# Optimization experiments

Measured on AMD Instinct MI355X. Metric: run time of the kernel, lower is better.

## Reference

```python
import jax, jax.numpy as jnp
import numpy as np

B, S, D_IN, D_OUT = 8, 2048, 1024, 64

def setup_inputs() -> dict:
    key = jax.random.key(0)
    ks = jax.random.split(key, 6)
    return {
        "inputs_for_keys": jax.random.normal(ks[0], (B, S, D_IN), jnp.float32),
        "inputs_for_values": jax.random.normal(ks[1], (B, S, D_IN), jnp.float32),
        "inputs_for_queries": jax.random.normal(ks[2], (B, S, D_IN), jnp.float32),
        "K": jax.random.normal(ks[3], (D_IN, D_OUT), jnp.float32) * (1.0 / np.sqrt(D_IN)),
        "V": jax.random.normal(ks[4], (D_IN, D_OUT), jnp.float32) * (1.0 / np.sqrt(D_IN)),
        "Q": jax.random.normal(ks[5], (D_IN, D_OUT), jnp.float32) * (1.0 / np.sqrt(D_IN)),
    }

def reference(inputs_for_keys, inputs_for_values, inputs_for_queries, K, V, Q):
    # Project to per-head key/value/query spaces: [B, S, D_OUT]
    keys = jnp.einsum('bsd,de->bse', inputs_for_keys, K)
    values = jnp.einsum('bsd,de->bse', inputs_for_values, V)
    queries = jnp.einsum('bsd,de->bse', inputs_for_queries, Q)
    d_k = keys.shape[-1]
    # Scaled dot-product scores: [B, Sq, Sk]
    score = jnp.einsum('bqe,bke->bqk', queries, keys) / jnp.sqrt(jnp.float32(d_k))
    # Causal mask: -inf strictly above the diagonal (query i attends to keys <= i)
    sq, sk = score.shape[1], score.shape[2]
    causal = jnp.triu(jnp.full((sq, sk), -jnp.inf, dtype=score.dtype), k=1)
    score = score + causal[None, :, :]
    weights = jax.nn.softmax(score, axis=-1)
    # Attention output: [B, Sq, D_OUT]
    return jnp.einsum('bqk,bke->bqe', weights, values)
```

## Files before the change

kernel.cpp:

```cpp
#include <hip/hip_runtime.h>
#include <stdint.h>

#define BB   8
#define SS   2048
#define DIN  1024
#define DOUT 64

typedef __bf16 bf16_t;
typedef __bf16 bf16x4 __attribute__((ext_vector_type(4)));
typedef __bf16 bf16x8 __attribute__((ext_vector_type(8)));
typedef float  f32x4  __attribute__((ext_vector_type(4)));
typedef unsigned int u32x4 __attribute__((ext_vector_type(4)));

#define LOG2E 1.44269504088896f

__device__ __forceinline__ void load_lds16(const void* g, void* l) {
    __builtin_amdgcn_global_load_lds(
        (const __attribute__((address_space(1))) void*)g,
        (__attribute__((address_space(3))) void*)l, 16, 0, 0);
}

__global__ void prep_weights(const float* __restrict__ Kw,
                             const float* __restrict__ Vw,
                             const float* __restrict__ Qw,
                             bf16_t* __restrict__ fw) {
    int proj = blockIdx.x >> 4;
    int seg  = blockIdx.x & 15;
    const float* W = (proj == 0) ? Kw : (proj == 1) ? Vw : Qw;
    float scale = (proj == 2) ? 0.125f : 1.0f;
    bf16_t* out = fw + proj * 65536;
    int base = seg * 4096;
#pragma unroll
    for (int i = 0; i < 16; ++i) {
        int idx  = base + i * 256 + threadIdx.x;
        int j    = idx & 7;
        int lane = (idx >> 3) & 63;
        int nt   = (idx >> 9) & 3;
        int kk   = idx >> 11;
        int k    = kk * 32 + (lane >> 4) * 8 + j;
        int col  = nt * 16 + (lane & 15);
        out[idx] = (bf16_t)(W[k * DOUT + col] * scale);
    }
}

__global__ __launch_bounds__(256) void proj_kernel(
    const float* __restrict__ Xk, const float* __restrict__ Xv,
    const float* __restrict__ Xq, const bf16_t* __restrict__ fw,
    bf16_t* __restrict__ outK, bf16_t* __restrict__ outVT,
    bf16_t* __restrict__ outQ) {
    __shared__ __align__(128) char Al[8192];
    __shared__ __align__(128) char Bl[8192];

    int tid  = threadIdx.x;
    int lane = tid & 63;
    int w    = tid >> 6;

    int proj = blockIdx.y;
    const float* X  = (proj == 0) ? Xk : (proj == 1) ? Xv : Xq;
    bf16_t* out     = (proj == 0) ? outK : (proj == 1) ? outVT : outQ;
    const bf16_t* fwp = fw + proj * 65536;

    int row0 = blockIdx.x * 32;

    const float* ga = X + (size_t)(row0 + (tid >> 4)) * DIN + ((tid & 15) ^ (tid >> 4)) * 4;
    char* alds0 = Al + (w << 10);
    char* alds1 = Al + 4096 + (w << 10);
    char* blds0 = Bl + (w << 10);
    char* blds1 = Bl + 4096 + (w << 10);

    f32x4 acc0 = (f32x4)(0.0f), acc1 = (f32x4)(0.0f);
    int r   = (w & 1) * 16 + (lane & 15);
    int nt0 = (w >> 1) * 2;

    for (int kt = 0; kt < 16; ++kt) {
        load_lds16(ga + kt * 64,               alds0);
        load_lds16(ga + 16 * DIN + kt * 64,    alds1);
        load_lds16(fwp + kt * 4096 + tid * 8,        blds0);
        load_lds16(fwp + kt * 4096 + 2048 + tid * 8, blds1);
        __syncthreads();

#pragma unroll
        for (int s = 0; s < 2; ++s) {
            int b0 = s * 8 + (lane >> 4) * 2;
            f32x4 lo = *(const f32x4*)(Al + r * 256 + (((b0    ) ^ (lane & 15)) << 4));
            f32x4 hi = *(const f32x4*)(Al + r * 256 + (((b0 + 1) ^ (lane & 15)) << 4));
            bf16x8 af;
            af[0] = (bf16_t)lo[0]; af[1] = (bf16_t)lo[1];
            af[2] = (bf16_t)lo[2]; af[3] = (bf16_t)lo[3];
            af[4] = (bf16_t)hi[0]; af[5] = (bf16_t)hi[1];
            af[6] = (bf16_t)hi[2]; af[7] = (bf16_t)hi[3];
            bf16x8 bf0 = *(const bf16x8*)(Bl + s * 4096 + nt0 * 1024 + lane * 16);
            bf16x8 bf1 = *(const bf16x8*)(Bl + s * 4096 + (nt0 + 1) * 1024 + lane * 16);
            acc0 = __builtin_amdgcn_mfma_f32_16x16x32_bf16(af, bf0, acc0, 0, 0, 0);
            acc1 = __builtin_amdgcn_mfma_f32_16x16x32_bf16(af, bf1, acc1, 0, 0, 0);
        }
        __syncthreads();
    }

    if (proj != 1) {
#pragma unroll
        for (int j = 0; j < 4; ++j) {
            int orow = row0 + (w & 1) * 16 + (lane >> 4) * 4 + j;
            out[(size_t)orow * DOUT + nt0 * 16 + (lane & 15)]       = (bf16_t)acc0[j];
            out[(size_t)orow * DOUT + (nt0 + 1) * 16 + (lane & 15)] = (bf16_t)acc1[j];
        }
    } else {
#pragma unroll
        for (int j = 0; j < 4; ++j) {
            int row = (w & 1) * 16 + (lane >> 4) * 4 + j;
            int c0  = nt0 * 16 + (lane & 15);
            int c1  = c0 + 16;
            *(bf16_t*)(Al + row * 128 + ((c0 * 2) ^ ((row & 7) << 4))) = (bf16_t)acc0[j];
            *(bf16_t*)(Al + row * 128 + ((c1 * 2) ^ ((row & 7) << 4))) = (bf16_t)acc1[j];
        }
        __syncthreads();
        int b  = row0 >> 11;
        int s0 = row0 & 2047;
        int sl = tid & 31;
        int d0 = (tid >> 5) * 8;
        bf16_t vals[8];
#pragma unroll
        for (int j = 0; j < 8; ++j)
            vals[j] = *(const bf16_t*)(Al + sl * 128 + (((d0 + j) * 2) ^ ((sl & 7) << 4)));
#pragma unroll
        for (int j = 0; j < 8; ++j)
            out[(size_t)b * (DOUT * SS) + (size_t)(d0 + j) * SS + s0 + sl] = vals[j];
    }
}

__global__ __launch_bounds__(256) void attn_kernel(
    const bf16_t* __restrict__ Kp, const bf16_t* __restrict__ VpT,
    const bf16_t* __restrict__ Qp, float* __restrict__ out,
    float* __restrict__ Opart, float* __restrict__ Oml, int split) {
    __shared__ __align__(16) char Plds[4][2048];

    int tid  = threadIdx.x;
    int lane = tid & 63;
    int w    = tid >> 6;
    int idx  = blockIdx.x;
    int b    = blockIdx.y;

    int qt, t0, t1, half = 0;
    bool partial;
    if (!split || idx < 16) { qt = idx; t0 = 0; t1 = qt + 1; partial = false; }
    else {
        int e = idx - 16;
        qt   = 16 + (e >> 1);
        half = e & 1;
        int T = qt + 1, h = (T + 1) >> 1;
        t0 = half ? h : 0;
        t1 = half ? T : h;
        partial = true;
    }

    const bf16_t* Kb = Kp  + (size_t)b * SS * DOUT;
    const bf16_t* Vb = VpT + (size_t)b * DOUT * SS;
    const bf16_t* Qb = Qp  + (size_t)b * SS * DOUT;

    bf16x8 aq0, aq1;
    {
        int rq = qt * 64 + w * 16 + (lane & 15);
        const bf16_t* qp = Qb + (size_t)rq * DOUT + (lane >> 4) * 8;
        aq0 = *(const bf16x8*)(qp);
        aq1 = *(const bf16x8*)(qp + 32);
    }

    float m[4], lsum[4];
    f32x4 acc[4];
#pragma unroll
    for (int r = 0; r < 4; ++r) { m[r] = -1e30f; lsum[r] = 0.0f; }
#pragma unroll
    for (int nt = 0; nt < 4; ++nt) acc[nt] = (f32x4)(0.0f);

    char* Pw = &Plds[w][0];

    for (int t = t0; t < t1; ++t) {
        f32x4 sfr[4];
#pragma unroll
        for (int nt = 0; nt < 4; ++nt) sfr[nt] = (f32x4)(0.0f);
#pragma unroll
        for (int kk = 0; kk < 2; ++kk) {
            int d0 = kk * 32 + (lane >> 4) * 8;
#pragma unroll
            for (int nt = 0; nt < 4; ++nt) {
                int key = nt * 16 + (lane & 15);
                bf16x8 bk = *(const bf16x8*)(Kb + (size_t)(t * 64 + key) * DOUT + d0);
                sfr[nt] = __builtin_amdgcn_mfma_f32_16x16x32_bf16(
                              kk == 0 ? aq0 : aq1, bk, sfr[nt], 0, 0, 0);
            }
        }

        if (t == qt) {
#pragma unroll
            for (int nt = 0; nt < 4; ++nt) {
                int key = nt * 16 + (lane & 15);
#pragma unroll
                for (int r = 0; r < 4; ++r) {
                    int q = w * 16 + (lane >> 4) * 4 + r;
                    if (key > q) sfr[nt][r] = -1e30f;
                }
            }
        }

        float pf[4][4];
#pragma unroll
        for (int r = 0; r < 4; ++r) {
            float mx = fmaxf(fmaxf(sfr[0][r], sfr[1][r]), fmaxf(sfr[2][r], sfr[3][r]));
            mx = fmaxf(mx, __shfl_xor(mx, 1));
            mx = fmaxf(mx, __shfl_xor(mx, 2));
            mx = fmaxf(mx, __shfl_xor(mx, 4));
            mx = fmaxf(mx, __shfl_xor(mx, 8));
            float mn = fmaxf(m[r], mx);
            float scale = exp2f((m[r] - mn) * LOG2E);
            m[r] = mn;
            float rs = 0.0f;
#pragma unroll
            for (int nt = 0; nt < 4; ++nt) {
                float p = exp2f((sfr[nt][r] - mn) * LOG2E);
                pf[nt][r] = p;
                rs += p;
            }
            rs += __shfl_xor(rs, 1);
            rs += __shfl_xor(rs, 2);
            rs += __shfl_xor(rs, 4);
            rs += __shfl_xor(rs, 8);
            lsum[r] = lsum[r] * scale + rs;
#pragma unroll
            for (int nt = 0; nt < 4; ++nt) acc[nt][r] *= scale;
        }

#pragma unroll
        for (int nt = 0; nt < 4; ++nt) {
            int key = nt * 16 + (lane & 15);
#pragma unroll
            for (int r = 0; r < 4; ++r) {
                int q = (lane >> 4) * 4 + r;
                *(bf16_t*)(Pw + q * 128 + ((key * 2) ^ ((q & 7) << 4))) = (bf16_t)pf[nt][r];
            }
        }

#pragma unroll
        for (int kk = 0; kk < 2; ++kk) {
            int k0 = kk * 32 + (lane >> 4) * 8;
            int q  = lane & 15;
            bf16x8 ap = *(const bf16x8*)(Pw + q * 128 + ((k0 * 2) ^ ((q & 7) << 4)));
#pragma unroll
            for (int nt = 0; nt < 4; ++nt) {
                int d = nt * 16 + (lane & 15);
                bf16x8 bv = *(const bf16x8*)(Vb + (size_t)d * SS + t * 64 + k0);
                acc[nt] = __builtin_amdgcn_mfma_f32_16x16x32_bf16(ap, bv, acc[nt], 0, 0, 0);
            }
        }
    }

    if (!partial) {
        float* ob = out + ((size_t)b * SS + qt * 64 + w * 16) * DOUT;
#pragma unroll
        for (int nt = 0; nt < 4; ++nt)
#pragma unroll
            for (int r = 0; r < 4; ++r) {
                int q = (lane >> 4) * 4 + r;
                int d = nt * 16 + (lane & 15);
                ob[(size_t)q * DOUT + d] = acc[nt][r] / lsum[r];
            }
    } else {
        size_t pbase = (((size_t)b * 16 + (qt - 16)) * 2 + half);
        float* Op = Opart + pbase * 4096;
        float* Ml = Oml   + pbase * 128;
#pragma unroll
        for (int nt = 0; nt < 4; ++nt)
#pragma unroll
            for (int r = 0; r < 4; ++r) {
                int row = w * 16 + (lane >> 4) * 4 + r;
                Op[row * 64 + nt * 16 + (lane & 15)] = acc[nt][r];
            }
        if ((lane & 15) == 0) {
#pragma unroll
            for (int r = 0; r < 4; ++r) {
                int row = w * 16 + (lane >> 4) * 4 + r;
                Ml[row * 2]     = m[r];
                Ml[row * 2 + 1] = lsum[r];
            }
        }
    }
}

__global__ __launch_bounds__(256) void attn_combine(
    const float* __restrict__ Opart, const float* __restrict__ Oml,
    float* __restrict__ out) {
    int qt  = 16 + blockIdx.x;
    int b   = blockIdx.y;
    int tid = threadIdx.x;
    int row = tid >> 2;
    int cb  = (tid & 3) * 16;

    size_t base = ((size_t)b * 16 + (qt - 16)) * 2;
    const float* O0 = Opart + base * 4096;
    const float* O1 = O0 + 4096;
    const float* M0 = Oml + base * 128;
    const float* M1 = M0 + 128;

    float m0 = M0[row * 2], l0 = M0[row * 2 + 1];
    float m1 = M1[row * 2], l1 = M1[row * 2 + 1];
    float mm = fmaxf(m0, m1);
    float e0 = exp2f((m0 - mm) * LOG2E);
    float e1 = exp2f((m1 - mm) * LOG2E);
    float li = 1.0f / (l0 * e0 + l1 * e1);

    const float* p0 = O0 + row * 64 + cb;
    const float* p1 = O1 + row * 64 + cb;
    float* ob = out + ((size_t)b * SS + qt * 64 + row) * DOUT + cb;
#pragma unroll
    for (int i = 0; i < 4; ++i) {
        f32x4 a = *(const f32x4*)(p0 + i * 4);
        f32x4 c = *(const f32x4*)(p1 + i * 4);
        f32x4 o;
#pragma unroll
        for (int j = 0; j < 4; ++j) o[j] = (a[j] * e0 + c[j] * e1) * li;
        *(f32x4*)(ob + i * 4) = o;
    }
}

extern "C" void kernel_launch(void* const* d_in, const int* in_sizes, int n_in,
                              void* d_out, int out_size, void* d_ws, size_t ws_size,
                              hipStream_t stream) {
    const float* Xk = (const float*)d_in[0];
    const float* Xv = (const float*)d_in[1];
    const float* Xq = (const float*)d_in[2];
    const float* Kw = (const float*)d_in[3];
    const float* Vw = (const float*)d_in[4];
    const float* Qw = (const float*)d_in[5];

    bf16_t* Kp  = (bf16_t*)d_ws;
    bf16_t* VpT = Kp  + (size_t)BB * SS * DOUT;
    bf16_t* Qp  = VpT + (size_t)BB * SS * DOUT;
    bf16_t* fw  = Qp  + (size_t)BB * SS * DOUT;
    char*   pend = (char*)(fw + 3 * 65536);
    float*  Opart = (float*)pend;
    float*  Oml   = Opart + (size_t)8 * 16 * 2 * 4096;

    size_t need = (size_t)((char*)(Oml + 8 * 16 * 2 * 128) - (char*)d_ws);
    int split = (ws_size >= need) ? 1 : 0;

    prep_weights<<<dim3(48), dim3(256), 0, stream>>>(Kw, Vw, Qw, fw);
    proj_kernel<<<dim3(512, 3), dim3(256), 0, stream>>>(Xk, Xv, Xq, fw, Kp, VpT, Qp);
    attn_kernel<<<dim3(split ? 48 : 32, 8), dim3(256), 0, stream>>>(
        Kp, VpT, Qp, (float*)d_out, Opart, Oml, split);
    if (split)
        attn_combine<<<dim3(16, 8), dim3(256), 0, stream>>>(Opart, Oml, (float*)d_out);
}
```

Before: 107.7 us.

## Triple-buffer projection GEMM LDS loads with manual vmcnt waits

Replaces the single-buffered load/sync/compute loop in the projection kernel with a 3-stage LDS ring buffer. Loads for tile t+2 are issued while tile t is computed, and explicit s_waitcnt vmcnt counts plus raw barriers replace __syncthreads. The goal is to hide global-memory latency of the fp32 activation stream behind the MFMA work. LDS use grows from 16KB to 48KB per block, which may reduce occupancy, and the hand-coded vmcnt values must match the number of outstanding loads.

```diff
diff --git a/kernel.cpp b/kernel.cpp
--- a/kernel.cpp
+++ b/kernel.cpp
@@ -48,8 +48,8 @@
     const float* __restrict__ Xq, const bf16_t* __restrict__ fw,
     bf16_t* __restrict__ outK, bf16_t* __restrict__ outVT,
     bf16_t* __restrict__ outQ) {
-    __shared__ __align__(128) char Al[8192];
-    __shared__ __align__(128) char Bl[8192];
+    __shared__ __align__(128) char Ab[3][8192];
+    __shared__ __align__(128) char Bb[3][8192];
 
     int tid  = threadIdx.x;
     int lane = tid & 63;
@@ -63,39 +63,51 @@
     int row0 = blockIdx.x * 32;
 
     const float* ga = X + (size_t)(row0 + (tid >> 4)) * DIN + ((tid & 15) ^ (tid >> 4)) * 4;
-    char* alds0 = Al + (w << 10);
-    char* alds1 = Al + 4096 + (w << 10);
-    char* blds0 = Bl + (w << 10);
-    char* blds1 = Bl + 4096 + (w << 10);
 
     f32x4 acc0 = (f32x4)(0.0f), acc1 = (f32x4)(0.0f);
     int r   = (w & 1) * 16 + (lane & 15);
     int nt0 = (w >> 1) * 2;
 
-    for (int kt = 0; kt < 16; ++kt) {
-        load_lds16(ga + kt * 64,               alds0);
-        load_lds16(ga + 16 * DIN + kt * 64,    alds1);
-        load_lds16(fwp + kt * 4096 + tid * 8,        blds0);
-        load_lds16(fwp + kt * 4096 + 2048 + tid * 8, blds1);
-        __syncthreads();
-
-#pragma unroll
-        for (int s = 0; s < 2; ++s) {
-            int b0 = s * 8 + (lane >> 4) * 2;
-            f32x4 lo = *(const f32x4*)(Al + r * 256 + (((b0    ) ^ (lane & 15)) << 4));
-            f32x4 hi = *(const f32x4*)(Al + r * 256 + (((b0 + 1) ^ (lane & 15)) << 4));
-            bf16x8 af;
-            af[0] = (bf16_t)lo[0]; af[1] = (bf16_t)lo[1];
-            af[2] = (bf16_t)lo[2]; af[3] = (bf16_t)lo[3];
-            af[4] = (bf16_t)hi[0]; af[5] = (bf16_t)hi[1];
-            af[6] = (bf16_t)hi[2]; af[7] = (bf16_t)hi[3];
-            bf16x8 bf0 = *(const bf16x8*)(Bl + s * 4096 + nt0 * 1024 + lane * 16);
-            bf16x8 bf1 = *(const bf16x8*)(Bl + s * 4096 + (nt0 + 1) * 1024 + lane * 16);
-            acc0 = __builtin_amdgcn_mfma_f32_16x16x32_bf16(af, bf0, acc0, 0, 0, 0);
-            acc1 = __builtin_amdgcn_mfma_f32_16x16x32_bf16(af, bf1, acc1, 0, 0, 0);
-        }
-        __syncthreads();
-    }
+#define STAGE(kt, b) do {                                                   \
+        load_lds16(ga + (kt) * 64,            Ab[b] + (w << 10));           \
+        load_lds16(ga + 16 * DIN + (kt) * 64, Ab[b] + 4096 + (w << 10));    \
+        load_lds16(fwp + (kt) * 4096 + tid * 8,        Bb[b] + (w << 10));  \
+        load_lds16(fwp + (kt) * 4096 + 2048 + tid * 8, Bb[b] + 4096 + (w << 10)); \
+    } while (0)
+
+#define COMPUTE(b) do {                                                     \
+        _Pragma("unroll")                                                   \
+        for (int s = 0; s < 2; ++s) {                                       \
+            int b0 = s * 8 + (lane >> 4) * 2;                               \
+            f32x4 lo = *(const f32x4*)(Ab[b] + r * 256 + (((b0    ) ^ (lane & 15)) << 4)); \
+            f32x4 hi = *(const f32x4*)(Ab[b] + r * 256 + (((b0 + 1) ^ (lane & 15)) << 4)); \
+            bf16x8 af;                                                      \
+            af[0] = (bf16_t)lo[0]; af[1] = (bf16_t)lo[1];                   \
+            af[2] = (bf16_t)lo[2]; af[3] = (bf16_t)lo[3];                   \
+            af[4] = (bf16_t)hi[0]; af[5] = (bf16_t)hi[1];                   \
+            af[6] = (bf16_t)hi[2]; af[7] = (bf16_t)hi[3];                   \
+            bf16x8 bf0 = *(const bf16x8*)(Bb[b] + s * 4096 + nt0 * 1024 + lane * 16); \
+            bf16x8 bf1 = *(const bf16x8*)(Bb[b] + s * 4096 + (nt0 + 1) * 1024 + lane * 16); \
+            acc0 = __builtin_amdgcn_mfma_f32_16x16x32_bf16(af, bf0, acc0, 0, 0, 0); \
+            acc1 = __builtin_amdgcn_mfma_f32_16x16x32_bf16(af, bf1, acc1, 0, 0, 0); \
+        }                                                                   \
+    } while (0)
+
+    STAGE(0, 0);
+    STAGE(1, 1);
+
+#pragma unroll
+    for (int t = 0; t < 16; ++t) {
+        if (t + 2 < 16) STAGE(t + 2, (t + 2) % 3);
+        if (t < 14)       asm volatile("s_waitcnt vmcnt(8)" ::: "memory");
+        else if (t == 14) asm volatile("s_waitcnt vmcnt(4)" ::: "memory");
+        else              asm volatile("s_waitcnt vmcnt(0)" ::: "memory");
+        __builtin_amdgcn_s_barrier();
+        COMPUTE(t % 3);
+        __builtin_amdgcn_s_barrier();
+    }
+#undef STAGE
+#undef COMPUTE
 
     if (proj != 1) {
 #pragma unroll
@@ -105,6 +117,7 @@
             out[(size_t)orow * DOUT + (nt0 + 1) * 16 + (lane & 15)] = (bf16_t)acc1[j];
         }
     } else {
+        char* Al = &Ab[0][0];
 #pragma unroll
         for (int j = 0; j < 4; ++j) {
             int row = (w & 1) * 16 + (lane >> 4) * 4 + j;
```

New measurement: 107.8 us. No clear change (+0.0%).
